# Kernel tuning notes

Measured on AMD Instinct MI355X. Metric: run time of the kernel, lower is better.

The kernel has to match this reference:

```python
import jax, jax.numpy as jnp
import numpy as np

B, T, C = 4, 128, 512
NH, HS = 8, 64          # n_head, head_dim = C // NH
ORDER = 3               # attention_order
SCALE = 1.0 / np.sqrt(HS)


def setup_inputs() -> dict:
    key = jax.random.key(0)
    ks = jax.random.split(key, 7)
    s = 0.02
    return {
        "x": jax.random.normal(ks[0], (B, T, C), jnp.float32),
        "Wp0": jax.random.normal(ks[1], (C, C), jnp.float32) * s,
        "Wp1": jax.random.normal(ks[2], (C, C), jnp.float32) * s,
        "Wp2": jax.random.normal(ks[3], (C, C), jnp.float32) * s,
        "Wv0": jax.random.normal(ks[4], (HS, HS), jnp.float32) * s,
        "Wv1": jax.random.normal(ks[5], (HS, HS), jnp.float32) * s,
        "Wc": jax.random.normal(ks[6], (C, C), jnp.float32) * s,
    }


def _heads(x, W):
    # Linear then split heads: (B,T,C) -> (B,NH,T,HS)
    return (x @ W).reshape(B, T, NH, HS).transpose(0, 2, 1, 3)


def _causal_mask(t, order):
    # indices grid [T]^order, True where i0 >= i1 >= ... >= i_{order-1}
    idx = jnp.arange(t)
    g = jnp.stack(jnp.meshgrid(*([idx] * order), indexing='ij'), axis=-1)
    return jnp.all(jnp.diff(g, axis=-1) <= 0, axis=-1)


def reference(x, Wp0, Wp1, Wp2, Wv0, Wv1, Wc):
    p0 = _heads(x, Wp0)  # (B,NH,T,HS)
    p1 = _heads(x, Wp1)
    p2 = _heads(x, Wp2)

    # pairwise scores, then higher-order broadcast exactly as the torch einsum
    # ('bh...i,bhkd->bh...ik' sums the key over d and broadcasts — faithful).
    att = jnp.einsum('bhid,bhjd->bhij', p0, p1) * SCALE        # (B,NH,T,T)
    att = jnp.einsum('bh...i,bhkd->bh...ik', att, p2)          # (B,NH,T,T,T)

    mask = _causal_mask(T, ORDER)[None, None]                  # (1,1,T,T,T)
    att = jnp.where(mask, att, -jnp.inf)
    att = jax.nn.softmax(att.reshape(B, NH, T, T * T), axis=-1)

    # value tensors with broadcasted elementwise product over the order dims
    V0 = (p1 @ Wv0)[:, :, :, None, :]   # (B,NH,T,1,HS)
    V1 = (p2 @ Wv1)[:, :, None, :, :]   # (B,NH,1,T,HS)
    V = (V0 * V1).reshape(B, NH, T * T, HS)

    y = jnp.einsum('bhij,bhjd->bhid', att, V)                  # (B,NH,T,HS)
    y = y.transpose(0, 2, 1, 3).reshape(B, T, C)
    return y @ Wc
```

## Files before the change

### kernel.cpp

```cpp
#include <hip/hip_runtime.h>
#include <hip/hip_bf16.h>
#include <math.h>

#define B 4
#define T 128
#define C 512
#define NH 8
#define HS 64
#define BH (B*NH)

typedef __attribute__((ext_vector_type(8))) short bf16x8;
typedef __attribute__((ext_vector_type(4))) float f32x4;

__device__ __forceinline__ unsigned short bfc(float x) {
    return __builtin_bit_cast(unsigned short, __float2bfloat16(x));
}
__device__ __forceinline__ float b2f(unsigned short u) {
    unsigned int x = ((unsigned int)u) << 16;
    return __builtin_bit_cast(float, x);
}
__device__ __forceinline__ unsigned int pk_bf16(float a, float b) {
    return (unsigned int)bfc(a) | ((unsigned int)bfc(b) << 16);
}

__global__ __launch_bounds__(256) void prep_kernel(
    const float* __restrict__ X, const float* __restrict__ Wp0, const float* __restrict__ Wp1,
    const float* __restrict__ Wp2, const float* __restrict__ Wc,
    const float* __restrict__ Wv0, const float* __restrict__ Wv1,
    unsigned short* __restrict__ Xb, unsigned short* __restrict__ W0T, unsigned short* __restrict__ W1T,
    unsigned short* __restrict__ W2T, unsigned short* __restrict__ WcT,
    unsigned short* __restrict__ We0T, unsigned short* __restrict__ We1T)
{
    __shared__ float Ls[64][69];
    __shared__ float As[16][68];
    __shared__ float Bs[16][68];
    const int z = blockIdx.z;
    const int tid = threadIdx.x;
    if (z == 0) {
        const int r0 = blockIdx.y * 64, c0 = blockIdx.x * 64;
        #pragma unroll
        for (int it = 0; it < 2; ++it) {
            const int q = tid + it * 256;
            const int row = q >> 3, c8 = (q & 7) * 8;
            const float4 a = *(const float4*)&X[(size_t)(r0 + row) * 512 + c0 + c8];
            const float4 b = *(const float4*)&X[(size_t)(r0 + row) * 512 + c0 + c8 + 4];
            uint4 o;
            o.x = pk_bf16(a.x, a.y);
            o.y = pk_bf16(a.z, a.w);
            o.z = pk_bf16(b.x, b.y);
            o.w = pk_bf16(b.z, b.w);
            *(uint4*)&Xb[(size_t)(r0 + row) * 512 + c0 + c8] = o;
        }
        return;
    }
    if (z <= 4) {
        const int r0 = blockIdx.y * 64, c0 = blockIdx.x * 64;
        const float* W = (z == 1) ? Wp0 : (z == 2) ? Wp1 : (z == 3) ? Wp2 : Wc;
        unsigned short* WT = (z == 1) ? W0T : (z == 2) ? W1T : (z == 3) ? W2T : WcT;
        #pragma unroll
        for (int it = 0; it < 4; ++it) {
            const int q = tid + it * 256;
            const int row = q >> 4, c4 = (q & 15) * 4;
            const float4 v = *(const float4*)&W[(size_t)(r0 + row) * 512 + c0 + c4];
            Ls[row][c4 + 0] = v.x; Ls[row][c4 + 1] = v.y; Ls[row][c4 + 2] = v.z; Ls[row][c4 + 3] = v.w;
        }
        __syncthreads();
        #pragma unroll
        for (int it = 0; it < 2; ++it) {
            const int q = tid + it * 256;
            const int nrow = q >> 3, k8 = (q & 7) * 8;
            uint4 o;
            o.x = pk_bf16(Ls[k8 + 0][nrow], Ls[k8 + 1][nrow]);
            o.y = pk_bf16(Ls[k8 + 2][nrow], Ls[k8 + 3][nrow]);
            o.z = pk_bf16(Ls[k8 + 4][nrow], Ls[k8 + 5][nrow]);
            o.w = pk_bf16(Ls[k8 + 6][nrow], Ls[k8 + 7][nrow]);
            *(uint4*)&WT[(size_t)(c0 + nrow) * 512 + r0 + k8] = o;
        }
        return;
    }
    const float* A  = (z == 5) ? Wp1 : Wp2;
    const float* Wv = (z == 5) ? Wv0 : Wv1;
    unsigned short* O = (z == 5) ? We0T : We1T;
    const int h = blockIdx.x;
    const int m0 = blockIdx.y * 64;
    const int tx = tid & 15, ty = tid >> 4;
    const int arow = tid >> 2, acol = (tid & 3) * 4;
    const int brow = tid >> 4, bcol = (tid & 15) * 4;
    float acc[4][4] = {};
    for (int k0 = 0; k0 < 64; k0 += 16) {
        const float4 av = *(const float4*)&A[(size_t)(m0 + arow) * 512 + h * 64 + k0 + acol];
        const float4 bv = *(const float4*)&Wv[(size_t)(k0 + brow) * 64 + bcol];
        __syncthreads();
        As[acol + 0][arow] = av.x; As[acol + 1][arow] = av.y;
        As[acol + 2][arow] = av.z; As[acol + 3][arow] = av.w;
        *(float4*)&Bs[brow][bcol] = bv;
        __syncthreads();
        #pragma unroll
        for (int kk = 0; kk < 16; ++kk) {
            const float4 a4 = *(const float4*)&As[kk][ty * 4];
            const float4 b4 = *(const float4*)&Bs[kk][tx * 4];
            const float ar[4] = {a4.x, a4.y, a4.z, a4.w};
            const float br[4] = {b4.x, b4.y, b4.z, b4.w};
            #pragma unroll
            for (int r = 0; r < 4; ++r)
                #pragma unroll
                for (int c = 0; c < 4; ++c)
                    acc[r][c] = fmaf(ar[r], br[c], acc[r][c]);
        }
    }
    #pragma unroll
    for (int r = 0; r < 4; ++r)
        #pragma unroll
        for (int c = 0; c < 4; ++c)
            O[(size_t)(h * 64 + tx * 4 + c) * 512 + (m0 + ty * 4 + r)] = bfc(acc[r][c]);
}

__global__ __launch_bounds__(256) void projmm_kernel(
    const unsigned short* __restrict__ Xb,
    const unsigned short* __restrict__ W0T, const unsigned short* __restrict__ W1T,
    const unsigned short* __restrict__ W2T,
    const unsigned short* __restrict__ We0T, const unsigned short* __restrict__ We1T,
    unsigned short* __restrict__ p0b, unsigned short* __restrict__ p1b,
    float* __restrict__ V0, unsigned short* __restrict__ V1T, float* __restrict__ rr)
{
    __shared__ __align__(16) unsigned short As[64][72];
    __shared__ __align__(16) unsigned short Bs[64][72];
    __shared__ float sRS[4][64];
    const int z = blockIdx.z;
    const unsigned short* WT = (z == 0) ? W0T : (z == 1) ? W1T : (z == 2) ? W2T : (z == 3) ? We0T : We1T;
    const int m0 = blockIdx.y * 64, n0 = blockIdx.x * 64;
    const int tid = threadIdx.x;
    const int w = tid >> 6, lane = tid & 63, quad = lane >> 4, l16 = lane & 15;
    f32x4 acc[4];
    #pragma unroll
    for (int mt = 0; mt < 4; ++mt) acc[mt] = (f32x4){0.f, 0.f, 0.f, 0.f};
    for (int k0 = 0; k0 < 512; k0 += 64) {
        __syncthreads();
        #pragma unroll
        for (int it = 0; it < 2; ++it) {
            const int q = tid + it * 256;
            const int row = q >> 3, c8 = (q & 7) * 8;
            *(uint4*)&As[row][c8] = *(const uint4*)&Xb[(size_t)(m0 + row) * 512 + k0 + c8];
            *(uint4*)&Bs[row][c8] = *(const uint4*)&WT[(size_t)(n0 + row) * 512 + k0 + c8];
        }
        __syncthreads();
        #pragma unroll
        for (int kt = 0; kt < 2; ++kt) {
            const bf16x8 b8 = *(const bf16x8*)&Bs[w * 16 + l16][kt * 32 + quad * 8];
            #pragma unroll
            for (int mt = 0; mt < 4; ++mt) {
                const bf16x8 a8 = *(const bf16x8*)&As[mt * 16 + l16][kt * 32 + quad * 8];
                acc[mt] = __builtin_amdgcn_mfma_f32_16x16x32_bf16(a8, b8, acc[mt], 0, 0, 0);
            }
        }
    }
    if (z == 2) {
        #pragma unroll
        for (int mt = 0; mt < 4; ++mt)
            #pragma unroll
            for (int r = 0; r < 4; ++r) {
                float v = acc[mt][r];
                v += __shfl_xor(v, 1, 64); v += __shfl_xor(v, 2, 64);
                v += __shfl_xor(v, 4, 64); v += __shfl_xor(v, 8, 64);
                if (l16 == 0) sRS[w][mt * 16 + quad * 4 + r] = v;
            }
        __syncthreads();
        if (tid < 64) {
            const float s = sRS[0][tid] + sRS[1][tid] + sRS[2][tid] + sRS[3][tid];
            const int m = m0 + tid, b = m >> 7, tl = m & 127, h = n0 >> 6;
            rr[(b * NH + h) * T + tl] = s;
        }
        return;
    }
    const int n = n0 + w * 16 + l16;
    const int h = n >> 6, d = n & 63;
    #pragma unroll
    for (int mt = 0; mt < 4; ++mt) {
        #pragma unroll
        for (int r = 0; r < 4; ++r) {
            const int m = m0 + mt * 16 + quad * 4 + r;
            const int b = m >> 7, t = m & 127;
            const size_t hm = (size_t)(b * NH + h) * T + t;
            const float v = acc[mt][r];
            if (z == 0)      p0b[hm * HS + d] = bfc(v);
            else if (z == 1) p1b[hm * HS + d] = bfc(v);
            else if (z == 3) V0[hm * HS + d] = v;
            else             V1T[((size_t)(b * NH + h) * HS + d) * T + t] = bfc(v);
        }
    }
}

__global__ __launch_bounds__(256) void attn_kernel(
    const unsigned short* __restrict__ p0b, const unsigned short* __restrict__ p1b,
    const float* __restrict__ rr, const float* __restrict__ V0g,
    const unsigned short* __restrict__ V1Tg, unsigned short* __restrict__ Yb)
{
    __shared__ __align__(16) unsigned short sE[128 * 128];
    __shared__ float sS[128];
    __shared__ float srr[128];
    __shared__ float sMS[4];
    __shared__ float sMR[4];
    __shared__ float sZ[4];

    const int blk = blockIdx.x;
    const int bh = blk & (BH - 1);
    const int i = (T - 1) - (blk >> 5);
    const int tid = threadIdx.x;
    const int w = tid >> 6;
    const int lane = tid & 63;
    const int quad = lane >> 4;
    const int l16 = lane & 15;

    if (tid < 128) srr[tid] = rr[bh * T + tid];

    uint4 v1r[4];
    {
        const unsigned short* src = V1Tg + ((size_t)bh * HS + (w << 4) + l16) * T + (quad << 3);
        #pragma unroll
        for (int kt = 0; kt < 4; ++kt) v1r[kt] = *(const uint4*)(src + (kt << 5));
    }

    {
        const unsigned short* ap = p0b + ((size_t)bh * T + i) * HS + (quad << 3);
        const unsigned short* bp = p1b + (size_t)bh * T * HS + (quad << 3);
        f32x4 s0 = (f32x4){0.f, 0.f, 0.f, 0.f};
        f32x4 s1 = (f32x4){0.f, 0.f, 0.f, 0.f};
        #pragma unroll
        for (int kt = 0; kt < 2; ++kt) {
            const bf16x8 a8 = *(const bf16x8*)(ap + (kt << 5));
            const bf16x8 b0 = *(const bf16x8*)(bp + (size_t)((w << 5) + l16) * HS + (kt << 5));
            const bf16x8 b1 = *(const bf16x8*)(bp + (size_t)((w << 5) + 16 + l16) * HS + (kt << 5));
            s0 = __builtin_amdgcn_mfma_f32_16x16x32_bf16(a8, b0, s0, 0, 0, 0);
            s1 = __builtin_amdgcn_mfma_f32_16x16x32_bf16(a8, b1, s1, 0, 0, 0);
        }
        if (quad == 0) {
            sS[(w << 5) + l16]      = s0[0] * 0.125f;
            sS[(w << 5) + 16 + l16] = s1[0] * 0.125f;
        }
    }
    __syncthreads();

    float aS = 0.f, aR = 0.f;
    if (tid <= i) {
        aS = fabsf(sS[tid]);
        aR = fabsf(srr[tid]);
    }
    #pragma unroll
    for (int off = 32; off; off >>= 1) {
        aS = fmaxf(aS, __shfl_xor(aS, off, 64));
        aR = fmaxf(aR, __shfl_xor(aR, off, 64));
    }
    if (lane == 0) { sMS[w] = aS; sMR[w] = aR; }

    const int cc = tid & 15;
    const int rowin = tid >> 4;
    float rk[8];
    __syncthreads();
    *(float4*)&rk[0] = *(const float4*)&srr[cc * 8];
    *(float4*)&rk[4] = *(const float4*)&srr[cc * 8 + 4];
    const float mS = fmaxf(fmaxf(sMS[0], sMS[1]), fmaxf(sMS[2], sMS[3]));
    const float mR = fmaxf(fmaxf(sMR[0], sMR[1]), fmaxf(sMR[2], sMR[3]));
    const float mhat = mS * mR;

    const float L2E = 1.4426950408889634f;
    const float bexp = -mhat * L2E;
    const int mtmax = i >> 4;
    float zacc = 0.f;
    for (int p = 0; p <= mtmax; ++p) {
        const int jj = (p << 4) + rowin;
        uint4 o = {0u, 0u, 0u, 0u};
        if (jj <= i && (cc << 3) <= jj) {
            const float aL = sS[jj] * L2E;
            const int dlim = jj - (cc << 3);
            float e[8];
            #pragma unroll
            for (int q = 0; q < 8; ++q) {
                const float ex = __builtin_amdgcn_exp2f(fmaf(aL, rk[q], bexp));
                e[q] = (q <= dlim) ? ex : 0.f;
                zacc += e[q];
            }
            o.x = pk_bf16(e[0], e[1]);
            o.y = pk_bf16(e[2], e[3]);
            o.z = pk_bf16(e[4], e[5]);
            o.w = pk_bf16(e[6], e[7]);
        }
        *(uint4*)((char*)sE + (jj << 8) + ((cc ^ (jj & 15)) << 4)) = o;
    }
    #pragma unroll
    for (int off = 32; off; off >>= 1) zacc += __shfl_xor(zacc, off, 64);
    if (lane == 0) sZ[w] = zacc;
    __syncthreads();
    const float Z = sZ[0] + sZ[1] + sZ[2] + sZ[3];

    f32x4 acc[8];
    #pragma unroll
    for (int mt = 0; mt < 8; ++mt) acc[mt] = (f32x4){0.f, 0.f, 0.f, 0.f};
    #pragma unroll
    for (int mt = 0; mt < 8; ++mt) {
        if (mt <= mtmax) {
            #pragma unroll
            for (int kt = 0; kt <= (mt >> 1); ++kt) {
                const int swz = (4 * kt + quad) ^ l16;
                const bf16x8 a8 = *(const bf16x8*)((char*)sE + (((mt << 4) + l16) << 8) + (swz << 4));
                acc[mt] = __builtin_amdgcn_mfma_f32_16x16x32_bf16(
                    a8, __builtin_bit_cast(bf16x8, v1r[kt]), acc[mt], 0, 0, 0);
            }
        }
    }

    const float* v0b = V0g + (size_t)bh * T * HS;
    const int d = (w << 4) + l16;
    float part = 0.f;
    #pragma unroll
    for (int mt = 0; mt < 8; ++mt) {
        if (mt < mtmax) {
            #pragma unroll
            for (int r = 0; r < 4; ++r) {
                const int jr = (mt << 4) + (quad << 2) + r;
                part = fmaf(v0b[jr * HS + d], acc[mt][r], part);
            }
        } else if (mt == mtmax) {
            #pragma unroll
            for (int r = 0; r < 4; ++r) {
                const int jr = (mt << 4) + (quad << 2) + r;
                if (jr <= i) part = fmaf(v0b[jr * HS + d], acc[mt][r], part);
            }
        }
    }
    part += __shfl_xor(part, 16, 64);
    part += __shfl_xor(part, 32, 64);
    if (lane < 16) {
        const int bb = bh >> 3, hh = bh & 7;
        Yb[((size_t)(bb * T + i) * C) + hh * HS + d] = bfc(part / Z);
    }
}

__global__ __launch_bounds__(256) void outmm_kernel(
    const unsigned short* __restrict__ Ab, const unsigned short* __restrict__ WT,
    float* __restrict__ OUT)
{
    __shared__ __align__(16) unsigned short As[64][72];
    __shared__ __align__(16) unsigned short Bs[64][72];
    const int m0 = blockIdx.y * 64, n0 = blockIdx.x * 64;
    const int tid = threadIdx.x;
    const int w = tid >> 6, lane = tid & 63, quad = lane >> 4, l16 = lane & 15;
    f32x4 acc[4];
    #pragma unroll
    for (int mt = 0; mt < 4; ++mt) acc[mt] = (f32x4){0.f, 0.f, 0.f, 0.f};
    for (int k0 = 0; k0 < 512; k0 += 64) {
        __syncthreads();
        #pragma unroll
        for (int it = 0; it < 2; ++it) {
            const int q = tid + it * 256;
            const int row = q >> 3, c8 = (q & 7) * 8;
            *(uint4*)&As[row][c8] = *(const uint4*)&Ab[(size_t)(m0 + row) * 512 + k0 + c8];
            *(uint4*)&Bs[row][c8] = *(const uint4*)&WT[(size_t)(n0 + row) * 512 + k0 + c8];
        }
        __syncthreads();
        #pragma unroll
        for (int kt = 0; kt < 2; ++kt) {
            const bf16x8 b8 = *(const bf16x8*)&Bs[w * 16 + l16][kt * 32 + quad * 8];
            #pragma unroll
            for (int mt = 0; mt < 4; ++mt) {
                const bf16x8 a8 = *(const bf16x8*)&As[mt * 16 + l16][kt * 32 + quad * 8];
                acc[mt] = __builtin_amdgcn_mfma_f32_16x16x32_bf16(a8, b8, acc[mt], 0, 0, 0);
            }
        }
    }
    const int n = n0 + w * 16 + l16;
    #pragma unroll
    for (int mt = 0; mt < 4; ++mt)
        #pragma unroll
        for (int r = 0; r < 4; ++r) {
            const int mrow = m0 + mt * 16 + quad * 4 + r;
            OUT[(size_t)mrow * 512 + n] = acc[mt][r];
        }
}

extern "C" void kernel_launch(void* const* d_in, const int* in_sizes, int n_in,
                              void* d_out, int out_size, void* d_ws, size_t ws_size,
                              hipStream_t stream)
{
    const float* x   = (const float*)d_in[0];
    const float* Wp0 = (const float*)d_in[1];
    const float* Wp1 = (const float*)d_in[2];
    const float* Wp2 = (const float*)d_in[3];
    const float* Wv0 = (const float*)d_in[4];
    const float* Wv1 = (const float*)d_in[5];
    const float* Wc  = (const float*)d_in[6];
    float* out = (float*)d_out;

    char* w8 = (char*)d_ws;
    const size_t HB = 512 * 1024;
    unsigned short* Xb   = (unsigned short*)(w8 + 0 * HB);
    unsigned short* W0T  = (unsigned short*)(w8 + 1 * HB);
    unsigned short* W1T  = (unsigned short*)(w8 + 2 * HB);
    unsigned short* W2T  = (unsigned short*)(w8 + 3 * HB);
    unsigned short* WcT  = (unsigned short*)(w8 + 4 * HB);
    unsigned short* We0T = (unsigned short*)(w8 + 5 * HB);
    unsigned short* We1T = (unsigned short*)(w8 + 6 * HB);
    unsigned short* p0b  = (unsigned short*)(w8 + 7 * HB);
    unsigned short* p1b  = (unsigned short*)(w8 + 8 * HB);
    float*          V0   = (float*)        (w8 + 9 * HB);
    unsigned short* V1T  = (unsigned short*)(w8 + 11 * HB);
    unsigned short* Yb   = (unsigned short*)(w8 + 12 * HB);
    float*          rr   = (float*)        (w8 + 13 * HB);

    prep_kernel  <<<dim3(8, 8, 7), 256, 0, stream>>>(x, Wp0, Wp1, Wp2, Wc, Wv0, Wv1,
                                                     Xb, W0T, W1T, W2T, WcT, We0T, We1T);
    projmm_kernel<<<dim3(8, 8, 5), 256, 0, stream>>>(Xb, W0T, W1T, W2T, We0T, We1T,
                                                     p0b, p1b, V0, V1T, rr);
    attn_kernel  <<<dim3(BH * T), 256, 0, stream>>>(p0b, p1b, rr, V0, V1T, Yb);
    outmm_kernel <<<dim3(8, 8), 256, 0, stream>>>(Yb, WcT, out);
}
```

Baseline: 122.9 us.

## Halve attention LDS tile with two-phase fill/MFMA and bf16 transposed V0

The attention kernel's exp tile in shared memory shrinks from 128x128 to 128x64 bf16. It is filled and consumed in two key halves, with a sync between each half, so more blocks can fit per CU. The max reduction now runs within a single wave, using shuffles instead of shared memory and a barrier. V0 is stored as transposed bf16 so each lane reads contiguous 8-byte vectors rather than strided fp32. The cost is extra barriers on long rows, and V0 loses precision from fp32 to bf16.

New measurement: 122.7 us. No clear change (-0.1%).

```diff
diff --git a/kernel.cpp b/kernel.cpp
--- a/kernel.cpp
+++ b/kernel.cpp
@@ -21,6 +21,12 @@
 }
 __device__ __forceinline__ unsigned int pk_bf16(float a, float b) {
     return (unsigned int)bfc(a) | ((unsigned int)bfc(b) << 16);
+}
+__device__ __forceinline__ float lo_f(unsigned int g) {
+    return __builtin_bit_cast(float, g << 16);
+}
+__device__ __forceinline__ float hi_f(unsigned int g) {
+    return __builtin_bit_cast(float, g & 0xffff0000u);
 }
 
 __global__ __launch_bounds__(256) void prep_kernel(
@@ -121,7 +127,7 @@
     const unsigned short* __restrict__ W2T,
     const unsigned short* __restrict__ We0T, const unsigned short* __restrict__ We1T,
     unsigned short* __restrict__ p0b, unsigned short* __restrict__ p1b,
-    float* __restrict__ V0, unsigned short* __restrict__ V1T, float* __restrict__ rr)
+    unsigned short* __restrict__ V0T, unsigned short* __restrict__ V1T, float* __restrict__ rr)
 {
     __shared__ __align__(16) unsigned short As[64][72];
     __shared__ __align__(16) unsigned short Bs[64][72];
@@ -184,7 +190,7 @@
             const float v = acc[mt][r];
             if (z == 0)      p0b[hm * HS + d] = bfc(v);
             else if (z == 1) p1b[hm * HS + d] = bfc(v);
-            else if (z == 3) V0[hm * HS + d] = v;
+            else if (z == 3) V0T[((size_t)(b * NH + h) * HS + d) * T + t] = bfc(v);
             else             V1T[((size_t)(b * NH + h) * HS + d) * T + t] = bfc(v);
         }
     }
@@ -192,14 +198,12 @@
 
 __global__ __launch_bounds__(256) void attn_kernel(
     const unsigned short* __restrict__ p0b, const unsigned short* __restrict__ p1b,
-    const float* __restrict__ rr, const float* __restrict__ V0g,
+    const float* __restrict__ rr, const unsigned short* __restrict__ V0Tg,
     const unsigned short* __restrict__ V1Tg, unsigned short* __restrict__ Yb)
 {
-    __shared__ __align__(16) unsigned short sE[128 * 128];
+    __shared__ __align__(16) unsigned short sE[128 * 64];
     __shared__ float sS[128];
     __shared__ float srr[128];
-    __shared__ float sMS[4];
-    __shared__ float sMR[4];
     __shared__ float sZ[4];
 
     const int blk = blockIdx.x;
@@ -240,38 +244,39 @@
     }
     __syncthreads();
 
-    float aS = 0.f, aR = 0.f;
-    if (tid <= i) {
-        aS = fabsf(sS[tid]);
-        aR = fabsf(srr[tid]);
-    }
-    #pragma unroll
-    for (int off = 32; off; off >>= 1) {
-        aS = fmaxf(aS, __shfl_xor(aS, off, 64));
-        aR = fmaxf(aR, __shfl_xor(aR, off, 64));
-    }
-    if (lane == 0) { sMS[w] = aS; sMR[w] = aR; }
-
-    const int cc = tid & 15;
-    const int rowin = tid >> 4;
-    float rk[8];
-    __syncthreads();
-    *(float4*)&rk[0] = *(const float4*)&srr[cc * 8];
-    *(float4*)&rk[4] = *(const float4*)&srr[cc * 8 + 4];
-    const float mS = fmaxf(fmaxf(sMS[0], sMS[1]), fmaxf(sMS[2], sMS[3]));
-    const float mR = fmaxf(fmaxf(sMR[0], sMR[1]), fmaxf(sMR[2], sMR[3]));
-    const float mhat = mS * mR;
+    float mhat;
+    {
+        float s0 = (lane <= i) ? fabsf(sS[lane]) : 0.f;
+        float s1 = (64 + lane <= i) ? fabsf(sS[64 + lane]) : 0.f;
+        float r0 = (lane <= i) ? fabsf(srr[lane]) : 0.f;
+        float r1 = (64 + lane <= i) ? fabsf(srr[64 + lane]) : 0.f;
+        float aS = fmaxf(s0, s1), aR = fmaxf(r0, r1);
+        #pragma unroll
+        for (int off = 32; off; off >>= 1) {
+            aS = fmaxf(aS, __shfl_xor(aS, off, 64));
+            aR = fmaxf(aR, __shfl_xor(aR, off, 64));
+        }
+        mhat = aS * aR;
+    }
 
     const float L2E = 1.4426950408889634f;
     const float bexp = -mhat * L2E;
     const int mtmax = i >> 4;
+    const int cc = tid & 7;
+    const int rowin = tid >> 3;
+    const int k0l = cc << 3;
     float zacc = 0.f;
-    for (int p = 0; p <= mtmax; ++p) {
-        const int jj = (p << 4) + rowin;
+
+    float rk[8];
+    *(float4*)&rk[0] = *(const float4*)&srr[k0l];
+    *(float4*)&rk[4] = *(const float4*)&srr[k0l + 4];
+    const int npass0 = (mtmax >> 1) + 1;
+    for (int p = 0; p < npass0; ++p) {
+        const int jj = (p << 5) + rowin;
         uint4 o = {0u, 0u, 0u, 0u};
-        if (jj <= i && (cc << 3) <= jj) {
+        if (jj <= i && k0l <= jj) {
             const float aL = sS[jj] * L2E;
-            const int dlim = jj - (cc << 3);
+            const int dlim = jj - k0l;
             float e[8];
             #pragma unroll
             for (int q = 0; q < 8; ++q) {
@@ -284,54 +289,117 @@
             o.z = pk_bf16(e[4], e[5]);
             o.w = pk_bf16(e[6], e[7]);
         }
-        *(uint4*)((char*)sE + (jj << 8) + ((cc ^ (jj & 15)) << 4)) = o;
-    }
-    #pragma unroll
-    for (int off = 32; off; off >>= 1) zacc += __shfl_xor(zacc, off, 64);
-    if (lane == 0) sZ[w] = zacc;
-    __syncthreads();
+        *(uint4*)&sE[(jj << 6) + ((cc ^ (jj & 7)) << 3)] = o;
+    }
+
+    f32x4 acc[8];
+    #pragma unroll
+    for (int mt = 0; mt < 8; ++mt) acc[mt] = (f32x4){0.f, 0.f, 0.f, 0.f};
+
+    if (mtmax < 4) {
+        #pragma unroll
+        for (int off = 32; off; off >>= 1) zacc += __shfl_xor(zacc, off, 64);
+        if (lane == 0) sZ[w] = zacc;
+        __syncthreads();
+        #pragma unroll
+        for (int mt = 0; mt < 4; ++mt) {
+            if (mt <= mtmax) {
+                #pragma unroll
+                for (int kt = 0; kt <= 1; ++kt) {
+                    if (kt <= (mt >> 1)) {
+                        const int swz = ((kt << 2) + quad) ^ (l16 & 7);
+                        const bf16x8 a8 = *(const bf16x8*)&sE[(((mt << 4) + l16) << 6) + (swz << 3)];
+                        acc[mt] = __builtin_amdgcn_mfma_f32_16x16x32_bf16(
+                            a8, __builtin_bit_cast(bf16x8, v1r[kt]), acc[mt], 0, 0, 0);
+                    }
+                }
+            }
+        }
+    } else {
+        __syncthreads();
+        #pragma unroll
+        for (int mt = 0; mt < 8; ++mt) {
+            if (mt <= mtmax) {
+                #pragma unroll
+                for (int kt = 0; kt <= 1; ++kt) {
+                    if (kt <= (mt >> 1)) {
+                        const int swz = ((kt << 2) + quad) ^ (l16 & 7);
+                        const bf16x8 a8 = *(const bf16x8*)&sE[(((mt << 4) + l16) << 6) + (swz << 3)];
+                        acc[mt] = __builtin_amdgcn_mfma_f32_16x16x32_bf16(
+                            a8, __builtin_bit_cast(bf16x8, v1r[kt]), acc[mt], 0, 0, 0);
+                    }
+                }
+            }
+        }
+        __syncthreads();
+        *(float4*)&rk[0] = *(const float4*)&srr[64 + k0l];
+        *(float4*)&rk[4] = *(const float4*)&srr[64 + k0l + 4];
+        const int npass1 = ((mtmax - 4) >> 1) + 1;
+        for (int p = 0; p < npass1; ++p) {
+            const int jj = 64 + (p << 5) + rowin;
+            uint4 o = {0u, 0u, 0u, 0u};
+            if (jj <= i && 64 + k0l <= jj) {
+                const float aL = sS[jj] * L2E;
+                const int dlim = jj - 64 - k0l;
+                float e[8];
+                #pragma unroll
+                for (int q = 0; q < 8; ++q) {
+                    const float ex = __builtin_amdgcn_exp2f(fmaf(aL, rk[q], bexp));
+                    e[q] = (q <= dlim) ? ex : 0.f;
+                    zacc += e[q];
+                }
+                o.x = pk_bf16(e[0], e[1]);
+                o.y = pk_bf16(e[2], e[3]);
+                o.z = pk_bf16(e[4], e[5]);
+                o.w = pk_bf16(e[6], e[7]);
+            }
+            *(uint4*)&sE[(jj << 6) + ((cc ^ (jj & 7)) << 3)] = o;
+        }
+        #pragma unroll
+        for (int off = 32; off; off >>= 1) zacc += __shfl_xor(zacc, off, 64);
+        if (lane == 0) sZ[w] = zacc;
+        __syncthreads();
+        #pragma unroll
+        for (int mt = 4; mt < 8; ++mt) {
+            if (mt <= mtmax) {
+                #pragma unroll
+                for (int kt = 2; kt <= 3; ++kt) {
+                    if (kt <= (mt >> 1)) {
+                        const int swz = (((kt & 1) << 2) + quad) ^ (l16 & 7);
+                        const bf16x8 a8 = *(const bf16x8*)&sE[(((mt << 4) + l16) << 6) + (swz << 3)];
+                        acc[mt] = __builtin_amdgcn_mfma_f32_16x16x32_bf16(
+                            a8, __builtin_bit_cast(bf16x8, v1r[kt]), acc[mt], 0, 0, 0);
+                    }
+                }
+            }
+        }
+    }
     const float Z = sZ[0] + sZ[1] + sZ[2] + sZ[3];
 
-    f32x4 acc[8];
-    #pragma unroll
-    for (int mt = 0; mt < 8; ++mt) acc[mt] = (f32x4){0.f, 0.f, 0.f, 0.f};
-    #pragma unroll
-    for (int mt = 0; mt < 8; ++mt) {
-        if (mt <= mtmax) {
-            #pragma unroll
-            for (int kt = 0; kt <= (mt >> 1); ++kt) {
-                const int swz = (4 * kt + quad) ^ l16;
-                const bf16x8 a8 = *(const bf16x8*)((char*)sE + (((mt << 4) + l16) << 8) + (swz << 4));
-                acc[mt] = __builtin_amdgcn_mfma_f32_16x16x32_bf16(
-                    a8, __builtin_bit_cast(bf16x8, v1r[kt]), acc[mt], 0, 0, 0);
-            }
-        }
-    }
-
-    const float* v0b = V0g + (size_t)bh * T * HS;
-    const int d = (w << 4) + l16;
+    const unsigned short* v0t = V0Tg + ((size_t)bh * HS + (w << 4) + l16) * T;
     float part = 0.f;
     #pragma unroll
     for (int mt = 0; mt < 8; ++mt) {
         if (mt < mtmax) {
-            #pragma unroll
-            for (int r = 0; r < 4; ++r) {
-                const int jr = (mt << 4) + (quad << 2) + r;
-                part = fmaf(v0b[jr * HS + d], acc[mt][r], part);
-            }
+            const uint2 u = *(const uint2*)&v0t[(mt << 4) + (quad << 2)];
+            part = fmaf(lo_f(u.x), acc[mt][0], part);
+            part = fmaf(hi_f(u.x), acc[mt][1], part);
+            part = fmaf(lo_f(u.y), acc[mt][2], part);
+            part = fmaf(hi_f(u.y), acc[mt][3], part);
         } else if (mt == mtmax) {
-            #pragma unroll
-            for (int r = 0; r < 4; ++r) {
-                const int jr = (mt << 4) + (quad << 2) + r;
-                if (jr <= i) part = fmaf(v0b[jr * HS + d], acc[mt][r], part);
-            }
+            const uint2 u = *(const uint2*)&v0t[(mt << 4) + (quad << 2)];
+            const int jb = (mt << 4) + (quad << 2);
+            if (jb + 0 <= i) part = fmaf(lo_f(u.x), acc[mt][0], part);
+            if (jb + 1 <= i) part = fmaf(hi_f(u.x), acc[mt][1], part);
+            if (jb + 2 <= i) part = fmaf(lo_f(u.y), acc[mt][2], part);
+            if (jb + 3 <= i) part = fmaf(hi_f(u.y), acc[mt][3], part);
         }
     }
     part += __shfl_xor(part, 16, 64);
     part += __shfl_xor(part, 32, 64);
     if (lane < 16) {
         const int bb = bh >> 3, hh = bh & 7;
-        Yb[((size_t)(bb * T + i) * C) + hh * HS + d] = bfc(part / Z);
+        Yb[((size_t)(bb * T + i) * C) + hh * HS + (w << 4) + l16] = bfc(part / Z);
     }
 }
 
@@ -401,15 +469,15 @@
     unsigned short* We1T = (unsigned short*)(w8 + 6 * HB);
     unsigned short* p0b  = (unsigned short*)(w8 + 7 * HB);
     unsigned short* p1b  = (unsigned short*)(w8 + 8 * HB);
-    float*          V0   = (float*)        (w8 + 9 * HB);
-    unsigned short* V1T  = (unsigned short*)(w8 + 11 * HB);
-    unsigned short* Yb   = (unsigned short*)(w8 + 12 * HB);
-    float*          rr   = (float*)        (w8 + 13 * HB);
+    unsigned short* V0T  = (unsigned short*)(w8 + 9 * HB);
+    unsigned short* V1T  = (unsigned short*)(w8 + 10 * HB);
+    unsigned short* Yb   = (unsigned short*)(w8 + 11 * HB);
+    float*          rr   = (float*)        (w8 + 12 * HB);
 
     prep_kernel  <<<dim3(8, 8, 7), 256, 0, stream>>>(x, Wp0, Wp1, Wp2, Wc, Wv0, Wv1,
                                                      Xb, W0T, W1T, W2T, WcT, We0T, We1T);
     projmm_kernel<<<dim3(8, 8, 5), 256, 0, stream>>>(Xb, W0T, W1T, W2T, We0T, We1T,
-                                                     p0b, p1b, V0, V1T, rr);
-    attn_kernel  <<<dim3(BH * T), 256, 0, stream>>>(p0b, p1b, rr, V0, V1T, Yb);
+                                                     p0b, p1b, V0T, V1T, rr);
+    attn_kernel  <<<dim3(BH * T), 256, 0, stream>>>(p0b, p1b, rr, V0T, V1T, Yb);
     outmm_kernel <<<dim3(8, 8), 256, 0, stream>>>(Yb, WcT, out);
 }
```
